# Performance work log

Hardware: AMD Instinct MI355X
Metric: run time of the kernel (lower is better)

Reference implementation:

```python
import jax, jax.numpy as jnp
import numpy as np

D_LOB = 128
D_HAWKES = 32
N_HEADS = 4
HEAD_DIM = D_LOB // N_HEADS
LN_EPS = 1e-5


def setup_inputs() -> dict:
    key = jax.random.key(0)
    ks = jax.random.split(key, 10)
    B, T = 8, 2048
    s = lambda fan_in: 1.0 / np.sqrt(fan_in)
    return {
        "lob": jax.random.normal(ks[0], (B, T, D_LOB), dtype=jnp.float32),
        "hawkes": jax.random.normal(ks[1], (B, T, D_HAWKES), dtype=jnp.float32),
        # hawkes_proj: Linear(d_hawkes, d_lob)
        "Wp": jax.random.uniform(ks[2], (D_LOB, D_HAWKES), jnp.float32, -s(D_HAWKES), s(D_HAWKES)),
        "bp": jnp.zeros((D_LOB,), jnp.float32),
        # MultiheadAttention packed in-projection (3*d_lob, d_lob) and out-projection
        "Win": jax.random.uniform(ks[3], (3 * D_LOB, D_LOB), jnp.float32, -s(D_LOB), s(D_LOB)),
        "bin_": jnp.zeros((3 * D_LOB,), jnp.float32),
        "Wo": jax.random.uniform(ks[4], (D_LOB, D_LOB), jnp.float32, -s(D_LOB), s(D_LOB)),
        "bo": jnp.zeros((D_LOB,), jnp.float32),
        # LayerNorm affine params
        "gamma": jnp.ones((D_LOB,), jnp.float32),
        "beta": jnp.zeros((D_LOB,), jnp.float32),
    }


def reference(lob, hawkes, Wp, bp, Win, bin_, Wo, bo, gamma, beta):
    B, T, _ = lob.shape
    # hawkes_proj
    h = hawkes @ Wp.T + bp  # (B, T, d_lob)
    # packed QKV projection (query=lob, key=value=h)
    q = lob @ Win[:D_LOB].T + bin_[:D_LOB]
    k = h @ Win[D_LOB:2 * D_LOB].T + bin_[D_LOB:2 * D_LOB]
    v = h @ Win[2 * D_LOB:].T + bin_[2 * D_LOB:]
    # split heads -> (B, H, T, hd)
    split = lambda x: x.reshape(B, T, N_HEADS, HEAD_DIM).transpose(0, 2, 1, 3)
    q, k, v = split(q), split(k), split(v)
    scale = 1.0 / np.sqrt(HEAD_DIM).astype(np.float32)
    scores = jnp.einsum("bhqd,bhkd->bhqk", q * scale, k)  # (B, H, T, T)
    attn = jax.nn.softmax(scores, axis=-1)
    # dropout(p=0.1) omitted: reference is eval/inference mode
    ctx = jnp.einsum("bhqk,bhkd->bhqd", attn, v)  # (B, H, T, hd)
    ctx = ctx.transpose(0, 2, 1, 3).reshape(B, T, D_LOB)
    fused = ctx @ Wo.T + bo
    # residual + LayerNorm
    x = lob + fused
    mu = jnp.mean(x, axis=-1, keepdims=True)
    var = jnp.mean(jnp.square(x - mu), axis=-1, keepdims=True)
    out = (x - mu) * jax.lax.rsqrt(var + LN_EPS) * gamma + beta
    attn_w = jnp.mean(attn, axis=1)  # average over heads (B, T, T)
    return out, attn_w
```

## Files before the change

### kernel.cpp

```cpp
#include <hip/hip_runtime.h>
#include <hip/hip_bf16.h>

#define TT 2048
#define BB 8
#define DD 128
#define HH 4
#define BT (BB*TT)
#define BH (BB*HH)
#define SCALE 0.1767766952966369f

typedef __attribute__((ext_vector_type(8))) short short8;
typedef __attribute__((ext_vector_type(4))) short s16x4;
typedef __attribute__((ext_vector_type(4))) float f32x4;
typedef __hip_bfloat16 bf16;

#define MFMA16(a,b,c) __builtin_amdgcn_mfma_f32_16x16x32_bf16(a,b,c,0,0,0)

static __device__ inline short8 ldg8(const bf16* p) {
  return *reinterpret_cast<const short8*>(p);
}
static __device__ inline float b2f(bf16 x) { return __bfloat162float(x); }
static __device__ inline short f2bs(float x) {
  bf16 h = __float2bfloat16(x);
  return *reinterpret_cast<short*>(&h);
}
static __device__ inline short8 ldcvt8(const float* p) {
  f32x4 f0 = *reinterpret_cast<const f32x4*>(p);
  f32x4 f1 = *reinterpret_cast<const f32x4*>(p + 4);
  short8 r;
  #pragma unroll
  for (int i = 0; i < 4; ++i) { r[i] = f2bs(f0[i]); r[4+i] = f2bs(f1[i]); }
  return r;
}

__global__ __launch_bounds__(256) void proj_kernel(
    const float* __restrict__ lob, const float* __restrict__ hawkes,
    const float* __restrict__ Wp, const float* __restrict__ bp,
    const float* __restrict__ Win, const float* __restrict__ binp,
    bf16* __restrict__ qg, bf16* __restrict__ kg, bf16* __restrict__ vtg) {
  __shared__ bf16 hT[32*136];
  __shared__ bf16 vT[128*40];
  int tid = threadIdx.x;
  int wave = tid >> 6, lane = tid & 63;
  int lr = lane & 15, lq = lane >> 4;
  int r0 = blockIdx.x * 32;
  int b  = r0 >> 11, t0 = r0 & 2047;
  f32x4 z = {0.f,0.f,0.f,0.f};

  short8 alob[2][4], ahk[2];
  #pragma unroll
  for (int mt = 0; mt < 2; ++mt) {
    const float* lp = lob + (size_t)(r0 + mt*16 + lr)*128;
    #pragma unroll
    for (int kt = 0; kt < 4; ++kt) alob[mt][kt] = ldcvt8(lp + kt*32 + lq*8);
    ahk[mt] = ldcvt8(hawkes + (size_t)(r0 + mt*16 + lr)*32 + lq*8);
  }

  for (int nt = wave; nt < 8; nt += 4) {
    int cn = nt*16;
    short8 bfrag = ldcvt8(Wp + (size_t)(cn + lr)*32 + lq*8);
    float bias = bp[cn + lr];
    #pragma unroll
    for (int mt = 0; mt < 2; ++mt) {
      f32x4 c = MFMA16(ahk[mt], bfrag, z);
      #pragma unroll
      for (int r = 0; r < 4; ++r)
        hT[(mt*16 + lq*4 + r)*136 + cn + lr] = __float2bfloat16(c[r] + bias);
    }
  }
  __syncthreads();

  short8 ah[2][4];
  #pragma unroll
  for (int mt = 0; mt < 2; ++mt)
    #pragma unroll
    for (int kt = 0; kt < 4; ++kt)
      ah[mt][kt] = *reinterpret_cast<const short8*>(&hT[(mt*16 + lr)*136 + kt*32 + lq*8]);

  for (int nt = wave; nt < 24; nt += 4) {
    int which = nt >> 3;
    int c = (nt & 7)*16 + lr;
    const float* wrow = Win + (size_t)(which*128 + c)*128;
    float bias = binp[which*128 + c];
    f32x4 acc0 = z, acc1 = z;
    #pragma unroll
    for (int kt = 0; kt < 4; ++kt) {
      short8 bfrag = ldcvt8(wrow + kt*32 + lq*8);
      if (which == 0) {
        acc0 = MFMA16(alob[0][kt], bfrag, acc0);
        acc1 = MFMA16(alob[1][kt], bfrag, acc1);
      } else {
        acc0 = MFMA16(ah[0][kt], bfrag, acc0);
        acc1 = MFMA16(ah[1][kt], bfrag, acc1);
      }
    }
    int head = c >> 5, dd = c & 31;
    #pragma unroll
    for (int mt = 0; mt < 2; ++mt) {
      f32x4 acc = mt ? acc1 : acc0;
      #pragma unroll
      for (int r = 0; r < 4; ++r) {
        int row = mt*16 + lq*4 + r;
        float val = acc[r] + bias;
        if (which == 0)
          qg[((size_t)(b*HH + head)*TT + t0 + row)*32 + dd] = __float2bfloat16(val * SCALE);
        else if (which == 1)
          kg[((size_t)(b*HH + head)*TT + t0 + row)*32 + dd] = __float2bfloat16(val);
        else
          vT[c*40 + row] = __float2bfloat16(val);
      }
    }
  }
  __syncthreads();

  {
    int dd = tid >> 1, half = tid & 1;
    int bh = b*HH + (dd >> 5);
    short8 s0 = *reinterpret_cast<const short8*>(&vT[dd*40 + half*16]);
    short8 s1 = *reinterpret_cast<const short8*>(&vT[dd*40 + half*16 + 8]);
    bf16* dst = vtg + ((size_t)bh*32 + (dd & 31))*TT + t0 + half*16;
    *reinterpret_cast<short8*>(dst) = s0;
    *reinterpret_cast<short8*>(dst + 8) = s1;
  }
}

__global__ __launch_bounds__(64) void lsum_kernel(const bf16* __restrict__ qg,
    const bf16* __restrict__ kg, float* __restrict__ lg) {
  int bh = blockIdx.x >> 6, qt = blockIdx.x & 63;
  int lane = threadIdx.x;
  int lr = lane & 15, lq = lane >> 4;
  const bf16* qp = qg + ((size_t)(bh*TT) + qt*32)*32;
  short8 a0 = ldg8(qp + lr*32 + lq*8);
  short8 a1 = ldg8(qp + (16+lr)*32 + lq*8);
  float rs[2][4] = {{0.f,0.f,0.f,0.f},{0.f,0.f,0.f,0.f}};
  for (int kt = 0; kt < 64; ++kt) {
    const bf16* kp = kg + ((size_t)(bh*TT) + kt*32)*32;
    short8 b0 = ldg8(kp + lr*32 + lq*8);
    short8 b1 = ldg8(kp + (16+lr)*32 + lq*8);
    f32x4 z = {0.f,0.f,0.f,0.f};
    f32x4 s00 = MFMA16(a0, b0, z);
    f32x4 s01 = MFMA16(a0, b1, z);
    f32x4 s10 = MFMA16(a1, b0, z);
    f32x4 s11 = MFMA16(a1, b1, z);
    #pragma unroll
    for (int r = 0; r < 4; ++r) {
      rs[0][r] += __expf(s00[r]) + __expf(s01[r]);
      rs[1][r] += __expf(s10[r]) + __expf(s11[r]);
    }
  }
  #pragma unroll
  for (int m = 1; m <= 8; m <<= 1) {
    #pragma unroll
    for (int mt = 0; mt < 2; ++mt)
      #pragma unroll
      for (int r = 0; r < 4; ++r)
        rs[mt][r] += __shfl_xor(rs[mt][r], m, 64);
  }
  if (lr == 0) {
    #pragma unroll
    for (int mt = 0; mt < 2; ++mt)
      #pragma unroll
      for (int r = 0; r < 4; ++r)
        lg[(size_t)bh*TT + qt*32 + mt*16 + lq*4 + r] = rs[mt][r];
  }
}

__global__ __launch_bounds__(256, 2) void attn_kernel(const bf16* __restrict__ qg,
    const bf16* __restrict__ kg, const bf16* __restrict__ vtg,
    const float* __restrict__ lg, float* __restrict__ attn_out,
    float* __restrict__ ctxg) {
  __shared__ __align__(16) char smem[20608];
  bf16*  pT   = (bf16*)smem;
  float* pred = (float*)smem;
  int tid = threadIdx.x;
  int wave = tid >> 6, lane = tid & 63;
  int lr = lane & 15, lq = lane >> 4;
  int qg2 = wave & 1, kh = wave >> 1;
  int r0 = blockIdx.x * 32;
  int b  = r0 >> 11;
  int t0 = (r0 & 2047) + qg2*16;
  f32x4 z = {0.f,0.f,0.f,0.f};

  short8 qf[4];
  float  rinv[4];
  #pragma unroll
  for (int h = 0; h < 4; ++h) {
    size_t bhT = (size_t)(b*HH + h)*TT;
    qf[h]   = ldg8(qg + (bhT + t0 + lr)*32 + lq*8);
    rinv[h] = 1.0f / lg[bhT + t0 + lr];
  }
  f32x4 acc[4][2];
  #pragma unroll
  for (int h = 0; h < 4; ++h) { acc[h][0] = z; acc[h][1] = z; }

  for (int kt = 0; kt < 32; ++kt) {
    int kb = kh*1024 + kt*32;
    __syncthreads();
    f32x4 m0 = z, m1 = z;
    #pragma unroll
    for (int h = 0; h < 4; ++h) {
      size_t bhT = (size_t)(b*HH + h)*TT;
      const bf16* kp = kg + (bhT + kb + lr)*32 + lq*8;
      short8 kf0 = ldg8(kp);
      short8 kf1 = ldg8(kp + 16*32);
      const bf16* vp = vtg + ((size_t)(b*HH + h)*32 + lr)*TT + kb + lq*8;
      short8 vf0 = ldg8(vp);
      short8 vf1 = ldg8(vp + (size_t)16*TT);
      f32x4 tt0 = MFMA16(kf0, qf[h], z);
      f32x4 tt1 = MFMA16(kf1, qf[h], z);
      f32x4 p0, p1;
      #pragma unroll
      for (int r = 0; r < 4; ++r) {
        p0[r] = __expf(tt0[r]) * rinv[h];
        p1[r] = __expf(tt1[r]) * rinv[h];
      }
      m0 += p0; m1 += p1;
      s16x4 w0, w1;
      #pragma unroll
      for (int r = 0; r < 4; ++r) { w0[r] = f2bs(p0[r]); w1[r] = f2bs(p1[r]); }
      bf16* pb = pT + wave*2560 + h*640 + lr*40;
      *reinterpret_cast<s16x4*>(pb + lq*4)      = w0;
      *reinterpret_cast<s16x4*>(pb + 16 + lq*4) = w1;
      short8 ap = *reinterpret_cast<const short8*>(pb + lq*8);
      acc[h][0] = MFMA16(ap, vf0, acc[h][0]);
      acc[h][1] = MFMA16(ap, vf1, acc[h][1]);
    }
    float* dst = attn_out + ((size_t)(b*TT) + t0 + lr)*TT + kb + lq*4;
    f32x4 s0 = m0 * 0.25f, s1 = m1 * 0.25f;
    *reinterpret_cast<f32x4*>(dst)      = s0;
    *reinterpret_cast<f32x4*>(dst + 16) = s1;
  }

  __syncthreads();
  if (kh == 1) {
    float* pr = pred + qg2*2112;
    #pragma unroll
    for (int h = 0; h < 4; ++h)
      #pragma unroll
      for (int nt = 0; nt < 2; ++nt)
        #pragma unroll
        for (int r = 0; r < 4; ++r)
          pr[(lq*4 + r)*132 + h*32 + nt*16 + lr] = acc[h][nt][r];
  }
  __syncthreads();
  if (kh == 0) {
    float* pr = pred + qg2*2112;
    #pragma unroll
    for (int h = 0; h < 4; ++h)
      #pragma unroll
      for (int nt = 0; nt < 2; ++nt)
        #pragma unroll
        for (int r = 0; r < 4; ++r) {
          float v = acc[h][nt][r] + pr[(lq*4 + r)*132 + h*32 + nt*16 + lr];
          ctxg[((size_t)(b*TT) + t0 + lq*4 + r)*128 + h*32 + nt*16 + lr] = v;
        }
  }
}

__global__ __launch_bounds__(256) void outln_kernel(const float* __restrict__ ctxg,
    const float* __restrict__ lob, const float* __restrict__ Wo,
    const float* __restrict__ bo, const float* __restrict__ gamma,
    const float* __restrict__ beta, float* __restrict__ outg) {
  __shared__ float sWo[128*129];
  __shared__ float sP[384];
  __shared__ float sCtx[4][128];
  __shared__ float sLob[4][128];
  int tid = threadIdx.x;
  for (int i = tid; i < 128*128; i += 256) {
    int c = i >> 7, d = i & 127;
    sWo[d*129 + c] = Wo[i];
  }
  if (tid < 128) {
    sP[tid] = bo[tid]; sP[128+tid] = gamma[tid]; sP[256+tid] = beta[tid];
  }
  __syncthreads();
  int wave = tid >> 6, lane = tid & 63;
  for (int it = 0; it < 8; ++it) {
    int row = blockIdx.x*32 + it*4 + wave;
    sCtx[wave][lane]    = ctxg[(size_t)row*128 + lane];
    sCtx[wave][64+lane] = ctxg[(size_t)row*128 + 64 + lane];
    sLob[wave][lane]    = lob[(size_t)row*128 + lane];
    sLob[wave][64+lane] = lob[(size_t)row*128 + 64 + lane];
    __syncthreads();
    float x0 = sP[lane] + sLob[wave][lane];
    float x1 = sP[64+lane] + sLob[wave][64+lane];
    #pragma unroll 8
    for (int d = 0; d < 128; ++d) {
      float cv = sCtx[wave][d];
      x0 += cv * sWo[d*129 + lane];
      x1 += cv * sWo[d*129 + 64 + lane];
    }
    float sum = x0 + x1;
    #pragma unroll
    for (int m = 1; m < 64; m <<= 1) sum += __shfl_xor(sum, m, 64);
    float mu = sum * (1.0f/128.0f);
    float d0 = x0 - mu, d1 = x1 - mu;
    float vs = d0*d0 + d1*d1;
    #pragma unroll
    for (int m = 1; m < 64; m <<= 1) vs += __shfl_xor(vs, m, 64);
    float rstd = rsqrtf(vs*(1.0f/128.0f) + 1e-5f);
    outg[(size_t)row*128 + lane]      = d0*rstd*sP[128+lane] + sP[256+lane];
    outg[(size_t)row*128 + 64 + lane] = d1*rstd*sP[192+lane] + sP[320+lane];
    __syncthreads();
  }
}

extern "C" void kernel_launch(void* const* d_in, const int* in_sizes, int n_in,
                              void* d_out, int out_size, void* d_ws, size_t ws_size,
                              hipStream_t stream) {
  const float* lob    = (const float*)d_in[0];
  const float* hawkes = (const float*)d_in[1];
  const float* Wp     = (const float*)d_in[2];
  const float* bp     = (const float*)d_in[3];
  const float* Win    = (const float*)d_in[4];
  const float* binp   = (const float*)d_in[5];
  const float* Wo     = (const float*)d_in[6];
  const float* bo     = (const float*)d_in[7];
  const float* gamma  = (const float*)d_in[8];
  const float* beta   = (const float*)d_in[9];
  float* outg = (float*)d_out;
  float* attn_out = outg + (size_t)BT*128;

  char* ws = (char*)d_ws;
  bf16*  qg   = (bf16*)(ws);
  bf16*  kg   = (bf16*)(ws + (size_t)4*1024*1024);
  bf16*  vtg  = (bf16*)(ws + (size_t)8*1024*1024);
  float* lg   = (float*)(ws + (size_t)12*1024*1024);
  float* ctxg = (float*)(ws + (size_t)12*1024*1024 + 512*1024);

  proj_kernel<<<BT/32, 256, 0, stream>>>(lob, hawkes, Wp, bp, Win, binp, qg, kg, vtg);
  lsum_kernel<<<BH*(TT/32), 64, 0, stream>>>(qg, kg, lg);
  attn_kernel<<<BT/32, 256, 0, stream>>>(qg, kg, vtg, lg, attn_out, ctxg);
  outln_kernel<<<512, 256, 0, stream>>>(ctxg, lob, Wo, bo, gamma, beta, outg);
}
```

Measured before the change: 332.3 us.

## Fuse softmax row-sum pass into attention kernel and software-pipeline PV

Removes the separate lsum kernel and computes the per-row exp sums inside the attention kernel, with each of four waves covering a quarter of the keys and combining the partials through shared memory. Blocks now cover 16 query rows, with waves split along the key dimension instead of query×key halves. The P tile is double-buffered so each P·V MFMA step runs one iteration behind the score computation, and the cross-wave ctx reduction now uses all four waves. This saves a launch and a global round trip for the sums, but recomputes QK^T in two passes per block, reloads Q per 16 rows, and raises shared memory use while targeting occupancy 3.

```diff
diff --git a/kernel.cpp b/kernel.cpp
--- a/kernel.cpp
+++ b/kernel.cpp
@@ -6,7 +6,6 @@
 #define DD 128
 #define HH 4
 #define BT (BB*TT)
-#define BH (BB*HH)
 #define SCALE 0.1767766952966369f
 
 typedef __attribute__((ext_vector_type(8))) short short8;
@@ -124,88 +123,70 @@
   }
 }
 
-__global__ __launch_bounds__(64) void lsum_kernel(const bf16* __restrict__ qg,
-    const bf16* __restrict__ kg, float* __restrict__ lg) {
-  int bh = blockIdx.x >> 6, qt = blockIdx.x & 63;
-  int lane = threadIdx.x;
-  int lr = lane & 15, lq = lane >> 4;
-  const bf16* qp = qg + ((size_t)(bh*TT) + qt*32)*32;
-  short8 a0 = ldg8(qp + lr*32 + lq*8);
-  short8 a1 = ldg8(qp + (16+lr)*32 + lq*8);
-  float rs[2][4] = {{0.f,0.f,0.f,0.f},{0.f,0.f,0.f,0.f}};
-  for (int kt = 0; kt < 64; ++kt) {
-    const bf16* kp = kg + ((size_t)(bh*TT) + kt*32)*32;
-    short8 b0 = ldg8(kp + lr*32 + lq*8);
-    short8 b1 = ldg8(kp + (16+lr)*32 + lq*8);
-    f32x4 z = {0.f,0.f,0.f,0.f};
-    f32x4 s00 = MFMA16(a0, b0, z);
-    f32x4 s01 = MFMA16(a0, b1, z);
-    f32x4 s10 = MFMA16(a1, b0, z);
-    f32x4 s11 = MFMA16(a1, b1, z);
-    #pragma unroll
-    for (int r = 0; r < 4; ++r) {
-      rs[0][r] += __expf(s00[r]) + __expf(s01[r]);
-      rs[1][r] += __expf(s10[r]) + __expf(s11[r]);
-    }
-  }
-  #pragma unroll
-  for (int m = 1; m <= 8; m <<= 1) {
-    #pragma unroll
-    for (int mt = 0; mt < 2; ++mt)
-      #pragma unroll
-      for (int r = 0; r < 4; ++r)
-        rs[mt][r] += __shfl_xor(rs[mt][r], m, 64);
-  }
-  if (lr == 0) {
-    #pragma unroll
-    for (int mt = 0; mt < 2; ++mt)
-      #pragma unroll
-      for (int r = 0; r < 4; ++r)
-        lg[(size_t)bh*TT + qt*32 + mt*16 + lq*4 + r] = rs[mt][r];
-  }
-}
-
-__global__ __launch_bounds__(256, 2) void attn_kernel(const bf16* __restrict__ qg,
+__global__ __launch_bounds__(256, 3) void attn_kernel(const bf16* __restrict__ qg,
     const bf16* __restrict__ kg, const bf16* __restrict__ vtg,
-    const float* __restrict__ lg, float* __restrict__ attn_out,
-    float* __restrict__ ctxg) {
-  __shared__ __align__(16) char smem[20608];
+    float* __restrict__ attn_out, float* __restrict__ ctxg) {
+  __shared__ __align__(16) char smem[41984];
   bf16*  pT   = (bf16*)smem;
+  float* slw  = (float*)(smem + 40960);
   float* pred = (float*)smem;
   int tid = threadIdx.x;
   int wave = tid >> 6, lane = tid & 63;
   int lr = lane & 15, lq = lane >> 4;
-  int qg2 = wave & 1, kh = wave >> 1;
-  int r0 = blockIdx.x * 32;
-  int b  = r0 >> 11;
-  int t0 = (r0 & 2047) + qg2*16;
+  int row0 = blockIdx.x * 16;
+  int b  = row0 >> 11, t0 = row0 & 2047;
   f32x4 z = {0.f,0.f,0.f,0.f};
 
   short8 qf[4];
-  float  rinv[4];
-  #pragma unroll
-  for (int h = 0; h < 4; ++h) {
-    size_t bhT = (size_t)(b*HH + h)*TT;
-    qf[h]   = ldg8(qg + (bhT + t0 + lr)*32 + lq*8);
-    rinv[h] = 1.0f / lg[bhT + t0 + lr];
-  }
-  f32x4 acc[4][2];
-  #pragma unroll
-  for (int h = 0; h < 4; ++h) { acc[h][0] = z; acc[h][1] = z; }
-
-  for (int kt = 0; kt < 32; ++kt) {
-    int kb = kh*1024 + kt*32;
-    __syncthreads();
-    f32x4 m0 = z, m1 = z;
+  #pragma unroll
+  for (int h = 0; h < 4; ++h)
+    qf[h] = ldg8(qg + ((size_t)(b*HH + h)*TT + t0 + lr)*32 + lq*8);
+
+  float ls[4] = {0.f,0.f,0.f,0.f};
+  for (int kt = 0; kt < 16; ++kt) {
+    int kb = wave*512 + kt*32;
     #pragma unroll
     for (int h = 0; h < 4; ++h) {
-      size_t bhT = (size_t)(b*HH + h)*TT;
-      const bf16* kp = kg + (bhT + kb + lr)*32 + lq*8;
+      const bf16* kp = kg + ((size_t)(b*HH + h)*TT + kb + lr)*32 + lq*8;
       short8 kf0 = ldg8(kp);
       short8 kf1 = ldg8(kp + 16*32);
-      const bf16* vp = vtg + ((size_t)(b*HH + h)*32 + lr)*TT + kb + lq*8;
-      short8 vf0 = ldg8(vp);
-      short8 vf1 = ldg8(vp + (size_t)16*TT);
+      f32x4 tt0 = MFMA16(kf0, qf[h], z);
+      f32x4 tt1 = MFMA16(kf1, qf[h], z);
+      #pragma unroll
+      for (int r = 0; r < 4; ++r) ls[h] += __expf(tt0[r]) + __expf(tt1[r]);
+    }
+  }
+  #pragma unroll
+  for (int h = 0; h < 4; ++h) {
+    ls[h] += __shfl_xor(ls[h], 16, 64);
+    ls[h] += __shfl_xor(ls[h], 32, 64);
+  }
+  if (lane < 16) {
+    #pragma unroll
+    for (int h = 0; h < 4; ++h) slw[(h*16 + lane)*4 + wave] = ls[h];
+  }
+  __syncthreads();
+  float rinv[4];
+  #pragma unroll
+  for (int h = 0; h < 4; ++h) {
+    f32x4 v = *reinterpret_cast<const f32x4*>(&slw[(h*16 + lr)*4]);
+    rinv[h] = 1.0f / (v[0] + v[1] + v[2] + v[3]);
+  }
+
+  f32x4 acc[4][2];
+  #pragma unroll
+  for (int h = 0; h < 4; ++h) { acc[h][0] = z; acc[h][1] = z; }
+  bf16* myP = pT + wave*5120;
+
+  auto computeP = [&](int kt) {
+    int kb = wave*512 + kt*32;
+    f32x4 m0 = z, m1 = z;
+    bf16* buf = myP + (kt & 1)*2560;
+    #pragma unroll
+    for (int h = 0; h < 4; ++h) {
+      const bf16* kp = kg + ((size_t)(b*HH + h)*TT + kb + lr)*32 + lq*8;
+      short8 kf0 = ldg8(kp);
+      short8 kf1 = ldg8(kp + 16*32);
       f32x4 tt0 = MFMA16(kf0, qf[h], z);
       f32x4 tt1 = MFMA16(kf1, qf[h], z);
       f32x4 p0, p1;
@@ -218,42 +199,56 @@
       s16x4 w0, w1;
       #pragma unroll
       for (int r = 0; r < 4; ++r) { w0[r] = f2bs(p0[r]); w1[r] = f2bs(p1[r]); }
-      bf16* pb = pT + wave*2560 + h*640 + lr*40;
+      bf16* pb = buf + h*640 + lr*40;
       *reinterpret_cast<s16x4*>(pb + lq*4)      = w0;
       *reinterpret_cast<s16x4*>(pb + 16 + lq*4) = w1;
-      short8 ap = *reinterpret_cast<const short8*>(pb + lq*8);
-      acc[h][0] = MFMA16(ap, vf0, acc[h][0]);
-      acc[h][1] = MFMA16(ap, vf1, acc[h][1]);
     }
     float* dst = attn_out + ((size_t)(b*TT) + t0 + lr)*TT + kb + lq*4;
     f32x4 s0 = m0 * 0.25f, s1 = m1 * 0.25f;
     *reinterpret_cast<f32x4*>(dst)      = s0;
     *reinterpret_cast<f32x4*>(dst + 16) = s1;
-  }
-
-  __syncthreads();
-  if (kh == 1) {
-    float* pr = pred + qg2*2112;
-    #pragma unroll
-    for (int h = 0; h < 4; ++h)
-      #pragma unroll
-      for (int nt = 0; nt < 2; ++nt)
-        #pragma unroll
-        for (int r = 0; r < 4; ++r)
-          pr[(lq*4 + r)*132 + h*32 + nt*16 + lr] = acc[h][nt][r];
-  }
-  __syncthreads();
-  if (kh == 0) {
-    float* pr = pred + qg2*2112;
-    #pragma unroll
-    for (int h = 0; h < 4; ++h)
-      #pragma unroll
-      for (int nt = 0; nt < 2; ++nt)
-        #pragma unroll
-        for (int r = 0; r < 4; ++r) {
-          float v = acc[h][nt][r] + pr[(lq*4 + r)*132 + h*32 + nt*16 + lr];
-          ctxg[((size_t)(b*TT) + t0 + lq*4 + r)*128 + h*32 + nt*16 + lr] = v;
-        }
+  };
+  auto doPV = [&](int kt) {
+    int kb = wave*512 + kt*32;
+    bf16* buf = myP + (kt & 1)*2560;
+    #pragma unroll
+    for (int h = 0; h < 4; ++h) {
+      const bf16* vp = vtg + ((size_t)(b*HH + h)*32 + lr)*TT + kb + lq*8;
+      short8 vf0 = ldg8(vp);
+      short8 vf1 = ldg8(vp + (size_t)16*TT);
+      short8 ap = *reinterpret_cast<const short8*>(buf + h*640 + lr*40 + lq*8);
+      acc[h][0] = MFMA16(ap, vf0, acc[h][0]);
+      acc[h][1] = MFMA16(ap, vf1, acc[h][1]);
+    }
+  };
+
+  computeP(0);
+  for (int kt = 1; kt < 16; ++kt) {
+    doPV(kt - 1);
+    computeP(kt);
+  }
+  doPV(15);
+
+  __syncthreads();
+  #pragma unroll
+  for (int h = 0; h < 4; ++h)
+    #pragma unroll
+    for (int nt = 0; nt < 2; ++nt)
+      #pragma unroll
+      for (int r = 0; r < 4; ++r)
+        pred[wave*2112 + (lq*4 + r)*132 + h*32 + nt*16 + lr] = acc[h][nt][r];
+  __syncthreads();
+  {
+    int q = tid >> 4, d0 = (tid & 15)*8;
+    f32x4 s0 = z, s1 = z;
+    #pragma unroll
+    for (int w = 0; w < 4; ++w) {
+      s0 += *reinterpret_cast<const f32x4*>(&pred[w*2112 + q*132 + d0]);
+      s1 += *reinterpret_cast<const f32x4*>(&pred[w*2112 + q*132 + d0 + 4]);
+    }
+    float* cdst = ctxg + ((size_t)(b*TT) + t0 + q)*128 + d0;
+    *reinterpret_cast<f32x4*>(cdst)     = s0;
+    *reinterpret_cast<f32x4*>(cdst + 4) = s1;
   }
 }
 
@@ -325,11 +320,9 @@
   bf16*  qg   = (bf16*)(ws);
   bf16*  kg   = (bf16*)(ws + (size_t)4*1024*1024);
   bf16*  vtg  = (bf16*)(ws + (size_t)8*1024*1024);
-  float* lg   = (float*)(ws + (size_t)12*1024*1024);
   float* ctxg = (float*)(ws + (size_t)12*1024*1024 + 512*1024);
 
   proj_kernel<<<BT/32, 256, 0, stream>>>(lob, hawkes, Wp, bp, Win, binp, qg, kg, vtg);
-  lsum_kernel<<<BH*(TT/32), 64, 0, stream>>>(qg, kg, lg);
-  attn_kernel<<<BT/32, 256, 0, stream>>>(qg, kg, vtg, lg, attn_out, ctxg);
+  attn_kernel<<<BT/16, 256, 0, stream>>>(qg, kg, vtg, attn_out, ctxg);
   outln_kernel<<<512, 256, 0, stream>>>(ctxg, lob, Wo, bo, gamma, beta, outg);
 }
```

Result: faster. 320.8 us (-3.4%).
